# Kernel optimization log

Measured on AMD Instinct MI355X. Metric: run time of the kernel, lower is better.

Reference implementation:

```python
import jax, jax.numpy as jnp
import numpy as np

HIDDEN = 1024
B, LQ, LK = 8, 2048, 2048


def setup_inputs() -> dict:
    key = jax.random.key(0)
    k1, k2, k3 = jax.random.split(key, 3)
    query = jax.random.normal(k1, (B, LQ, HIDDEN), dtype=jnp.float32)
    key_t = jax.random.normal(k2, (B, LK, HIDDEN), dtype=jnp.float32)
    # multiplicative binary mask on scores (float 0/1)
    attention_mask = jax.random.randint(k3, (B, LQ, LK), 0, 2).astype(jnp.float32)
    return {"query": query, "key": key_t, "attention_mask": attention_mask}


def reference(query, key, attention_mask):
    sqrt_dim = np.sqrt(HIDDEN).astype(np.float32)
    # [B, Lq, Lk] scores, scaled then multiplicatively masked (NOT additive)
    score = jnp.einsum("bqd,bkd->bqk", query, key) / sqrt_dim
    score = score * attention_mask
    attn = jax.nn.softmax(score, axis=-1)
    # NOTE: original module multiplies attn by KEY (not value)
    context = jnp.einsum("bqk,bkd->bqd", attn, key)
    return (context, attn)
```

## Files before the change

kernel.cpp:

```cpp
#include <hip/hip_runtime.h>
#include <hip/hip_bf16.h>


typedef __attribute__((ext_vector_type(8))) short bf16x8;
typedef __attribute__((ext_vector_type(4))) float f32x4;
typedef __attribute__((ext_vector_type(4))) unsigned u32x4;
typedef __attribute__((ext_vector_type(2))) unsigned u32x2;

constexpr int BATCH = 8;
constexpr int LQ    = 2048;
constexpr int LKK   = 2048;
constexpr int DH    = 1024;
constexpr float SCALE = 0.03125f;

#define GAS(p) ((const __attribute__((address_space(1))) void*)(p))
#define LAS(p) ((__attribute__((address_space(3))) void*)(p))

__device__ __forceinline__ unsigned lds_addr(const unsigned short* p) {
    return (unsigned)(unsigned long long)
        (const __attribute__((address_space(3))) unsigned short*)p;
}

__device__ __forceinline__ bf16x8 dsr_b128(unsigned off) {
    bf16x8 r;
    asm volatile("ds_read_b128 %0, %1" : "=v"(r) : "v"(off));
    return r;
}

__device__ __forceinline__ unsigned pack_bf16x2(float x0, float x1) {
    unsigned a = __builtin_bit_cast(unsigned, x0) + 0x8000u;
    unsigned b = __builtin_bit_cast(unsigned, x1) + 0x8000u;
    return __builtin_amdgcn_perm(b, a, 0x07060302u);
}

__global__ __launch_bounds__(256)
void cvt_kernel(const float* __restrict__ Q, const float* __restrict__ K,
                unsigned short* __restrict__ Qb, unsigned short* __restrict__ Kb) {
    const int bid = blockIdx.x;
    const float* src; unsigned short* dst; size_t off;
    if (bid < 4096) { src = Q; dst = Qb; off = (size_t)bid * 4096; }
    else            { src = K; dst = Kb; off = (size_t)(bid - 4096) * 4096; }
    off += (size_t)threadIdx.x * 16;
    const f32x4 a = *(const f32x4*)(src + off);
    const f32x4 b = *(const f32x4*)(src + off + 4);
    const f32x4 c = *(const f32x4*)(src + off + 8);
    const f32x4 d = *(const f32x4*)(src + off + 12);
    u32x4 v0, v1;
    v0[0] = pack_bf16x2(a[0], a[1]); v0[1] = pack_bf16x2(a[2], a[3]);
    v0[2] = pack_bf16x2(b[0], b[1]); v0[3] = pack_bf16x2(b[2], b[3]);
    v1[0] = pack_bf16x2(c[0], c[1]); v1[1] = pack_bf16x2(c[2], c[3]);
    v1[2] = pack_bf16x2(d[0], d[1]); v1[3] = pack_bf16x2(d[2], d[3]);
    *(u32x4*)(dst + off)     = v0;
    *(u32x4*)(dst + off + 8) = v1;
}

__global__ __launch_bounds__(256)
void kt_kernel(const float* __restrict__ K, unsigned short* __restrict__ KT) {
    const int b  = blockIdx.z;
    const int k0 = blockIdx.y * 64;
    const int d0 = blockIdx.x * 64;
    const int t  = threadIdx.x;
    const int k4 = (t >> 4) * 4;
    const int d4 = (t & 15) * 4;
    f32x4 rk[4];
    const float* Kp = K + ((size_t)b * LKK + k0 + k4) * DH + d0 + d4;
#pragma unroll
    for (int j = 0; j < 4; ++j) rk[j] = *(const f32x4*)(Kp + (size_t)j * DH);
    unsigned short* Tp = KT + ((size_t)b * DH + d0 + d4) * LKK + k0 + k4;
#pragma unroll
    for (int c = 0; c < 4; ++c) {
        u32x2 w;
        w[0] = pack_bf16x2(rk[0][c], rk[1][c]);
        w[1] = pack_bf16x2(rk[2][c], rk[3][c]);
        *(u32x2*)(Tp + (size_t)c * LKK) = w;
    }
}

template<int LDA, int LDB, int NT>
__device__ __forceinline__ void gemm8_mainloop(
    const unsigned short* __restrict__ Ab,
    const unsigned short* __restrict__ Bb,
    unsigned short* lA, unsigned short* lB,
    f32x4 (&acc)[8][4])
{
    const int tid  = threadIdx.x;
    const int lane = tid & 63;
    const int wid  = tid >> 6;
    const int wm   = (wid & 1) * 128;
    const int wn   = (wid >> 1) * 64;
    const int lrow = lane & 15;
    const int quad = lane >> 4;
    const int slotsw = (quad ^ ((lrow >> 1) & 3)) * 8;

    const int srow0 = wid * 32 + (lane >> 2);
    const int srow1 = srow0 + 16;
    const int sc    = ((lane & 3) ^ ((lane >> 3) & 3)) * 8;

    auto stage = [&](int I) {
        const int tile = I >> 2;
        const int h    = I & 3;
        const int kh   = h >> 1;
        const int kb   = tile * 64 + kh * 32 + sc;
        const unsigned short* s = (h & 1) ? Bb : Ab;
        const int ld            = (h & 1) ? LDB : LDA;
        unsigned short* d = ((h & 1) ? lB : lA)
                          + (tile & 1) * 16384 + kh * 8192 + wid * 1024;
        __builtin_amdgcn_global_load_lds(GAS(s + (size_t)srow0 * ld + kb), LAS(d),       16, 0, 0);
        __builtin_amdgcn_global_load_lds(GAS(s + (size_t)srow1 * ld + kb), LAS(d + 512), 16, 0, 0);
    };

#pragma unroll
    for (int i = 0; i < 8; ++i)
#pragma unroll
        for (int j = 0; j < 4; ++j) acc[i][j] = (f32x4){0.f, 0.f, 0.f, 0.f};

#pragma unroll
    for (int I = 0; I < 6; ++I) stage(I);
    asm volatile("s_waitcnt vmcnt(4)" ::: "memory");
    __builtin_amdgcn_s_barrier();

    for (int T = 0; T < NT; ++T) {
        const int par = (T & 1) * 16384;
        bf16x8 bfr[4];
#pragma unroll
        for (int q = 0; q < 4; ++q) {
            const int kh = (q >> 1) * 8192;
            const int mh = (q & 1) * 4;
            if ((q & 1) == 0) {
#pragma unroll
                for (int nf = 0; nf < 4; ++nf)
                    bfr[nf] = dsr_b128(lds_addr(&lB[par + kh + (wn + nf * 16 + lrow) * 32 + slotsw]));
            }
            bf16x8 af[4];
#pragma unroll
            for (int mf = 0; mf < 4; ++mf)
                af[mf] = dsr_b128(lds_addr(&lA[par + kh + (wm + (mh + mf) * 16 + lrow) * 32 + slotsw]));

            if (4 * T + q + 6 < 4 * NT) stage(4 * T + q + 6);

            __builtin_amdgcn_s_barrier();
            asm volatile("s_waitcnt lgkmcnt(0)" ::: "memory");
            __builtin_amdgcn_sched_barrier(0);
            __builtin_amdgcn_s_setprio(1);
#pragma unroll
            for (int mf = 0; mf < 4; ++mf)
#pragma unroll
                for (int nf = 0; nf < 4; ++nf)
                    acc[mh + mf][nf] = __builtin_amdgcn_mfma_f32_16x16x32_bf16(
                        af[mf], bfr[nf], acc[mh + mf][nf], 0, 0, 0);
            __builtin_amdgcn_s_setprio(0);
            if (q == 3) {
                if (T < NT - 2)       asm volatile("s_waitcnt vmcnt(4)" ::: "memory");
                else if (T == NT - 2) asm volatile("s_waitcnt vmcnt(0)" ::: "memory");
            }
            __builtin_amdgcn_s_barrier();
        }
    }
}

__global__ __launch_bounds__(512, 2)
void qk8(const unsigned short* __restrict__ Qb, const unsigned short* __restrict__ Kb,
         const float* __restrict__ M, float* __restrict__ S) {
    __shared__ __align__(16) unsigned short lA[32768];
    __shared__ __align__(16) unsigned short lB[32768];

    const int l   = blockIdx.x;
    const int swz = (l & 7) * 64 + (l >> 3);
    const int b   = swz >> 6;
    const int my  = (swz >> 3) & 7;
    const int nx  = swz & 7;
    const int q0  = my * 256;
    const int n0  = nx * 256;

    const unsigned short* Ap = Qb + ((size_t)b * LQ  + q0) * DH;
    const unsigned short* Bp = Kb + ((size_t)b * LKK + n0) * DH;

    f32x4 acc[8][4];
    gemm8_mainloop<DH, DH, DH / 64>(Ap, Bp, lA, lB, acc);

    const int lane = threadIdx.x & 63;
    const int wid  = threadIdx.x >> 6;
    const int wm   = (wid & 1) * 128;
    const int wn   = (wid >> 1) * 64;
    const int lrow = lane & 15;
    const int quad = lane >> 4;

    const size_t base = (size_t)b * LQ * LKK;
#pragma unroll
    for (int mf = 0; mf < 8; ++mf) {
#pragma unroll
        for (int r = 0; r < 4; ++r) {
            const int row = q0 + wm + mf * 16 + quad * 4 + r;
            const size_t rb = base + (size_t)row * LKK;
#pragma unroll
            for (int nf = 0; nf < 4; ++nf) {
                const int col = n0 + wn + nf * 16 + lrow;
                S[rb + col] = acc[mf][nf][r] * SCALE * M[rb + col];
            }
        }
    }
}

__global__ __launch_bounds__(256)
void softmax_kernel(float* __restrict__ A, unsigned short* __restrict__ ab) {
    float* p = A + (size_t)blockIdx.x * LKK;
    const int tid  = threadIdx.x;
    const int lane = tid & 63;
    const int wid  = tid >> 6;

    f32x4 v0 = *(const f32x4*)(p + tid * 8);
    f32x4 v1 = *(const f32x4*)(p + tid * 8 + 4);

    float m = v0[0];
#pragma unroll
    for (int i = 1; i < 4; ++i) m = fmaxf(m, v0[i]);
#pragma unroll
    for (int i = 0; i < 4; ++i) m = fmaxf(m, v1[i]);
#pragma unroll
    for (int o = 32; o >= 1; o >>= 1) m = fmaxf(m, __shfl_xor(m, o, 64));

    __shared__ float red[8];
    if (lane == 0) red[wid] = m;
    __syncthreads();
    m = fmaxf(fmaxf(red[0], red[1]), fmaxf(red[2], red[3]));

    float s = 0.f;
    f32x4 e0, e1;
#pragma unroll
    for (int i = 0; i < 4; ++i) { e0[i] = __expf(v0[i] - m); s += e0[i]; }
#pragma unroll
    for (int i = 0; i < 4; ++i) { e1[i] = __expf(v1[i] - m); s += e1[i]; }
#pragma unroll
    for (int o = 32; o >= 1; o >>= 1) s += __shfl_xor(s, o, 64);
    if (lane == 0) red[4 + wid] = s;
    __syncthreads();
    const float inv = 1.f / (red[4] + red[5] + red[6] + red[7]);

#pragma unroll
    for (int i = 0; i < 4; ++i) { e0[i] *= inv; e1[i] *= inv; }
    *(f32x4*)(p + tid * 8)     = e0;
    *(f32x4*)(p + tid * 8 + 4) = e1;

    if (ab) {
        u32x4 w;
        w[0] = pack_bf16x2(e0[0], e0[1]); w[1] = pack_bf16x2(e0[2], e0[3]);
        w[2] = pack_bf16x2(e1[0], e1[1]); w[3] = pack_bf16x2(e1[2], e1[3]);
        *(u32x4*)(ab + (size_t)blockIdx.x * LKK + tid * 8) = w;
    }
}

__global__ __launch_bounds__(512, 2)
void pk8(const unsigned short* __restrict__ Pb, const unsigned short* __restrict__ KT,
         float* __restrict__ C) {
    __shared__ __align__(16) unsigned short lA[32768];
    __shared__ __align__(16) unsigned short lB[32768];

    const int l   = blockIdx.x;
    const int swz = (l & 7) * 32 + (l >> 3);
    const int b   = swz >> 5;
    const int my  = (swz >> 2) & 7;
    const int nx  = swz & 3;
    const int q0  = my * 256;
    const int n0  = nx * 256;

    const unsigned short* Ap = Pb + ((size_t)b * LQ + q0) * LKK;
    const unsigned short* Bp = KT + ((size_t)b * DH + n0) * LKK;

    f32x4 acc[8][4];
    gemm8_mainloop<LKK, LKK, LKK / 64>(Ap, Bp, lA, lB, acc);

    const int lane = threadIdx.x & 63;
    const int wid  = threadIdx.x >> 6;
    const int wm   = (wid & 1) * 128;
    const int wn   = (wid >> 1) * 64;
    const int lrow = lane & 15;
    const int quad = lane >> 4;

    const size_t cb = (size_t)b * LQ * DH;
#pragma unroll
    for (int mf = 0; mf < 8; ++mf) {
#pragma unroll
        for (int r = 0; r < 4; ++r) {
            const int row = q0 + wm + mf * 16 + quad * 4 + r;
            const size_t rbase = cb + (size_t)row * DH;
#pragma unroll
            for (int nf = 0; nf < 4; ++nf)
                C[rbase + n0 + wn + nf * 16 + lrow] = acc[mf][nf][r];
        }
    }
}

constexpr int BM = 128, BN = 128, TK = 32;
constexpr int LDSS = 40;
__global__ __launch_bounds__(256, 2)
void pk_kernel(const float* __restrict__ P, const float* __restrict__ K,
               float* __restrict__ C) {
    __shared__ unsigned short lA[BM * LDSS];
    __shared__ unsigned short lB[BN * LDSS];

    const int b  = blockIdx.z;
    const int q0 = blockIdx.y * BM;
    const int n0 = blockIdx.x * BN;
    const float* Pp = P + (size_t)b * LQ * LKK + (size_t)q0 * LKK;
    const float* Kb = K + (size_t)b * LKK * DH;

    const int tid  = threadIdx.x;
    const int lane = tid & 63;
    const int wid  = tid >> 6;
    const int wm   = (wid & 1) * 64;
    const int wn   = (wid >> 1) * 64;
    const int lrow = lane & 15;
    const int quad = lane >> 4;

    f32x4 acc[4][4];
#pragma unroll
    for (int i = 0; i < 4; ++i)
#pragma unroll
        for (int j = 0; j < 4; ++j) acc[i][j] = (f32x4){0.f, 0.f, 0.f, 0.f};

    const int srow = tid >> 3;
    const int skq  = (tid & 7) << 2;
    const int tdb  = tid >> 3;
    const int tkb  = tid & 7;

    for (int k0 = 0; k0 < LKK; k0 += TK) {
        __syncthreads();
#pragma unroll
        for (int i = 0; i < 4; ++i) {
            const int row = i * 32 + srow;
            const f32x4 va = *(const f32x4*)(Pp + (size_t)row * LKK + k0 + skq);
            unsigned* pa = (unsigned*)&lA[row * LDSS + skq];
            pa[0] = pack_bf16x2(va[0], va[1]);
            pa[1] = pack_bf16x2(va[2], va[3]);
        }
        f32x4 rk[4];
#pragma unroll
        for (int j = 0; j < 4; ++j)
            rk[j] = *(const f32x4*)(Kb + (size_t)(k0 + tkb * 4 + j) * DH + n0 + tdb * 4);
#pragma unroll
        for (int c = 0; c < 4; ++c) {
            unsigned* pb = (unsigned*)&lB[(tdb * 4 + c) * LDSS + tkb * 4];
            pb[0] = pack_bf16x2(rk[0][c], rk[1][c]);
            pb[1] = pack_bf16x2(rk[2][c], rk[3][c]);
        }
        __syncthreads();

        bf16x8 af[4], bfr[4];
#pragma unroll
        for (int i = 0; i < 4; ++i) {
            af[i]  = *(const bf16x8*)&lA[(wm + i * 16 + lrow) * LDSS + quad * 8];
            bfr[i] = *(const bf16x8*)&lB[(wn + i * 16 + lrow) * LDSS + quad * 8];
        }
#pragma unroll
        for (int i = 0; i < 4; ++i)
#pragma unroll
            for (int j = 0; j < 4; ++j)
                acc[i][j] = __builtin_amdgcn_mfma_f32_16x16x32_bf16(af[i], bfr[j], acc[i][j], 0, 0, 0);
    }

    const size_t cb = (size_t)b * LQ * DH;
#pragma unroll
    for (int i = 0; i < 4; ++i) {
#pragma unroll
        for (int r = 0; r < 4; ++r) {
            const int row = q0 + wm + i * 16 + quad * 4 + r;
            const size_t rbase = cb + (size_t)row * DH;
#pragma unroll
            for (int j = 0; j < 4; ++j)
                C[rbase + n0 + wn + j * 16 + lrow] = acc[i][j][r];
        }
    }
}

extern "C" void kernel_launch(void* const* d_in, const int* in_sizes, int n_in,
                              void* d_out, int out_size, void* d_ws, size_t ws_size,
                              hipStream_t stream) {
    const float* Q = (const float*)d_in[0];
    const float* K = (const float*)d_in[1];
    const float* M = (const float*)d_in[2];

    constexpr size_t QEL  = (size_t)BATCH * LQ * DH;
    constexpr size_t AEL  = (size_t)BATCH * LQ * LKK;
    constexpr size_t KTEL = (size_t)BATCH * DH * LKK;

    float* ctx  = (float*)d_out;
    float* attn = ctx + QEL;

    unsigned short* Qb = (unsigned short*)ctx;
    unsigned short* Kb = Qb + QEL;

    const bool wsOK = ws_size >= (KTEL + AEL) * sizeof(unsigned short);
    unsigned short* KT = (unsigned short*)d_ws;
    unsigned short* ab = KT + KTEL;

    cvt_kernel<<<dim3(8192), 256, 0, stream>>>(Q, K, Qb, Kb);
    if (wsOK)
        kt_kernel<<<dim3(DH / 64, LKK / 64, BATCH), 256, 0, stream>>>(K, KT);
    qk8<<<dim3(BATCH * (LQ / 256) * (LKK / 256)), 512, 0, stream>>>(Qb, Kb, M, attn);
    softmax_kernel<<<dim3(BATCH * LQ), 256, 0, stream>>>(attn, wsOK ? ab : nullptr);
    if (wsOK)
        pk8<<<dim3(BATCH * (LQ / 256) * (DH / 256)), 512, 0, stream>>>(ab, KT, ctx);
    else
        pk_kernel<<<dim3(DH / BN, LQ / BM, BATCH), 256, 0, stream>>>(attn, K, ctx);
}
```

Measured before the change: 562.8 us.

## Deepen GEMM prefetch, stage K transpose via LDS, use one wave per softmax row

The K transpose kernel now stages its tile through LDS so each thread writes KT with coalesced 16-byte stores instead of scattered 8-byte stores. The shared GEMM main loop prefetches further ahead (up to two extra stage loads per tile, waitcnt thresholds raised), and it is unrolled in pairs so LDS buffer offsets are compile-time constants. The softmax gives each row to a single wavefront, removing the LDS reductions and __syncthreads, and launches a quarter as many blocks. The deeper prefetch costs more in-flight loads and registers, and the waitcnt bookkeeping becomes harder to get right.

```diff
diff --git a/kernel.cpp b/kernel.cpp
--- a/kernel.cpp
+++ b/kernel.cpp
@@ -56,6 +56,7 @@
 
 __global__ __launch_bounds__(256)
 void kt_kernel(const float* __restrict__ K, unsigned short* __restrict__ KT) {
+    __shared__ unsigned short T[64 * 68];
     const int b  = blockIdx.z;
     const int k0 = blockIdx.y * 64;
     const int d0 = blockIdx.x * 64;
@@ -66,14 +67,25 @@
     const float* Kp = K + ((size_t)b * LKK + k0 + k4) * DH + d0 + d4;
 #pragma unroll
     for (int j = 0; j < 4; ++j) rk[j] = *(const f32x4*)(Kp + (size_t)j * DH);
-    unsigned short* Tp = KT + ((size_t)b * DH + d0 + d4) * LKK + k0 + k4;
 #pragma unroll
     for (int c = 0; c < 4; ++c) {
         u32x2 w;
         w[0] = pack_bf16x2(rk[0][c], rk[1][c]);
         w[1] = pack_bf16x2(rk[2][c], rk[3][c]);
-        *(u32x2*)(Tp + (size_t)c * LKK) = w;
-    }
+        *(u32x2*)&T[(d4 + c) * 68 + k4] = w;
+    }
+    __syncthreads();
+    const int d  = t >> 2;
+    const int kc = (t & 3) * 16;
+    u32x2 a0 = *(const u32x2*)&T[d * 68 + kc];
+    u32x2 a1 = *(const u32x2*)&T[d * 68 + kc + 4];
+    u32x2 a2 = *(const u32x2*)&T[d * 68 + kc + 8];
+    u32x2 a3 = *(const u32x2*)&T[d * 68 + kc + 12];
+    unsigned short* dst = KT + ((size_t)b * DH + d0 + d) * LKK + k0 + kc;
+    u32x4 w0; w0[0] = a0[0]; w0[1] = a0[1]; w0[2] = a1[0]; w0[3] = a1[1];
+    u32x4 w1; w1[0] = a2[0]; w1[1] = a2[1]; w1[2] = a3[0]; w1[3] = a3[1];
+    *(u32x4*)dst       = w0;
+    *(u32x4*)(dst + 8) = w1;
 }
 
 template<int LDA, int LDB, int NT>
@@ -97,6 +109,7 @@
     const int sc    = ((lane & 3) ^ ((lane >> 3) & 3)) * 8;
 
     auto stage = [&](int I) {
+        if (I >= 4 * NT) return;
         const int tile = I >> 2;
         const int h    = I & 3;
         const int kh   = h >> 1;
@@ -116,11 +129,10 @@
 
 #pragma unroll
     for (int I = 0; I < 6; ++I) stage(I);
-    asm volatile("s_waitcnt vmcnt(4)" ::: "memory");
+    asm volatile("s_waitcnt vmcnt(8)" ::: "memory");
     __builtin_amdgcn_s_barrier();
 
-    for (int T = 0; T < NT; ++T) {
-        const int par = (T & 1) * 16384;
+    auto tilebody = [&](int T, int par) {
         bf16x8 bfr[4];
 #pragma unroll
         for (int q = 0; q < 4; ++q) {
@@ -136,7 +148,9 @@
             for (int mf = 0; mf < 4; ++mf)
                 af[mf] = dsr_b128(lds_addr(&lA[par + kh + (wm + (mh + mf) * 16 + lrow) * 32 + slotsw]));
 
-            if (4 * T + q + 6 < 4 * NT) stage(4 * T + q + 6);
+            if (q == 0)      stage(4 * T + 6);
+            else if (q == 1) stage(4 * T + 7);
+            else if (q == 2) { stage(4 * T + 8); stage(4 * T + 9); }
 
             __builtin_amdgcn_s_barrier();
             asm volatile("s_waitcnt lgkmcnt(0)" ::: "memory");
@@ -149,12 +163,20 @@
                     acc[mh + mf][nf] = __builtin_amdgcn_mfma_f32_16x16x32_bf16(
                         af[mf], bfr[nf], acc[mh + mf][nf], 0, 0, 0);
             __builtin_amdgcn_s_setprio(0);
-            if (q == 3) {
-                if (T < NT - 2)       asm volatile("s_waitcnt vmcnt(4)" ::: "memory");
-                else if (T == NT - 2) asm volatile("s_waitcnt vmcnt(0)" ::: "memory");
+            if (q == 1) {
+                if (T < NT - 1)      asm volatile("s_waitcnt vmcnt(8)" ::: "memory");
+                else                 asm volatile("s_waitcnt vmcnt(0)" ::: "memory");
+            } else if (q == 3) {
+                if (T < NT - 2)      asm volatile("s_waitcnt vmcnt(8)" ::: "memory");
+                else if (T == NT - 2) asm volatile("s_waitcnt vmcnt(4)" ::: "memory");
             }
             __builtin_amdgcn_s_barrier();
         }
+    };
+
+    for (int T = 0; T < NT; T += 2) {
+        tilebody(T,     0);
+        tilebody(T + 1, 16384);
     }
 }
 
@@ -203,49 +225,47 @@
 
 __global__ __launch_bounds__(256)
 void softmax_kernel(float* __restrict__ A, unsigned short* __restrict__ ab) {
-    float* p = A + (size_t)blockIdx.x * LKK;
-    const int tid  = threadIdx.x;
-    const int lane = tid & 63;
-    const int wid  = tid >> 6;
-
-    f32x4 v0 = *(const f32x4*)(p + tid * 8);
-    f32x4 v1 = *(const f32x4*)(p + tid * 8 + 4);
-
-    float m = v0[0];
-#pragma unroll
-    for (int i = 1; i < 4; ++i) m = fmaxf(m, v0[i]);
-#pragma unroll
-    for (int i = 0; i < 4; ++i) m = fmaxf(m, v1[i]);
+    const int row  = blockIdx.x * 4 + (threadIdx.x >> 6);
+    const int lane = threadIdx.x & 63;
+    float* p = A + (size_t)row * LKK;
+
+    f32x4 v[8];
+#pragma unroll
+    for (int i = 0; i < 8; ++i) v[i] = *(const f32x4*)(p + i * 256 + lane * 4);
+
+    float m = v[0][0];
+#pragma unroll
+    for (int i = 0; i < 8; ++i)
+#pragma unroll
+        for (int j = 0; j < 4; ++j) m = fmaxf(m, v[i][j]);
 #pragma unroll
     for (int o = 32; o >= 1; o >>= 1) m = fmaxf(m, __shfl_xor(m, o, 64));
 
-    __shared__ float red[8];
-    if (lane == 0) red[wid] = m;
-    __syncthreads();
-    m = fmaxf(fmaxf(red[0], red[1]), fmaxf(red[2], red[3]));
-
     float s = 0.f;
-    f32x4 e0, e1;
-#pragma unroll
-    for (int i = 0; i < 4; ++i) { e0[i] = __expf(v0[i] - m); s += e0[i]; }
-#pragma unroll
-    for (int i = 0; i < 4; ++i) { e1[i] = __expf(v1[i] - m); s += e1[i]; }
+#pragma unroll
+    for (int i = 0; i < 8; ++i)
+#pragma unroll
+        for (int j = 0; j < 4; ++j) { v[i][j] = __expf(v[i][j] - m); s += v[i][j]; }
 #pragma unroll
     for (int o = 32; o >= 1; o >>= 1) s += __shfl_xor(s, o, 64);
-    if (lane == 0) red[4 + wid] = s;
-    __syncthreads();
-    const float inv = 1.f / (red[4] + red[5] + red[6] + red[7]);
-
-#pragma unroll
-    for (int i = 0; i < 4; ++i) { e0[i] *= inv; e1[i] *= inv; }
-    *(f32x4*)(p + tid * 8)     = e0;
-    *(f32x4*)(p + tid * 8 + 4) = e1;
+    const float inv = 1.f / s;
+
+#pragma unroll
+    for (int i = 0; i < 8; ++i) {
+#pragma unroll
+        for (int j = 0; j < 4; ++j) v[i][j] *= inv;
+        *(f32x4*)(p + i * 256 + lane * 4) = v[i];
+    }
 
     if (ab) {
-        u32x4 w;
-        w[0] = pack_bf16x2(e0[0], e0[1]); w[1] = pack_bf16x2(e0[2], e0[3]);
-        w[2] = pack_bf16x2(e1[0], e1[1]); w[3] = pack_bf16x2(e1[2], e1[3]);
-        *(u32x4*)(ab + (size_t)blockIdx.x * LKK + tid * 8) = w;
+        unsigned short* q = ab + (size_t)row * LKK;
+#pragma unroll
+        for (int i = 0; i < 8; ++i) {
+            u32x2 w;
+            w[0] = pack_bf16x2(v[i][0], v[i][1]);
+            w[1] = pack_bf16x2(v[i][2], v[i][3]);
+            *(u32x2*)(q + i * 256 + lane * 4) = w;
+        }
     }
 }
 
@@ -397,7 +417,7 @@
     if (wsOK)
         kt_kernel<<<dim3(DH / 64, LKK / 64, BATCH), 256, 0, stream>>>(K, KT);
     qk8<<<dim3(BATCH * (LQ / 256) * (LKK / 256)), 512, 0, stream>>>(Qb, Kb, M, attn);
-    softmax_kernel<<<dim3(BATCH * LQ), 256, 0, stream>>>(attn, wsOK ? ab : nullptr);
+    softmax_kernel<<<dim3(BATCH * LQ / 4), 256, 0, stream>>>(attn, wsOK ? ab : nullptr);
     if (wsOK)
         pk8<<<dim3(BATCH * (LQ / 256) * (DH / 256)), 512, 0, stream>>>(ab, KT, ctx);
     else
```

After: 574.7 us. 1.02x slower.
